# Optimization experiments

Measured on AMD Instinct MI355X. Metric: run time of the kernel, lower is better.

## Reference

```python
import jax, jax.numpy as jnp
import numpy as np

EPS = 1e-6      # delta in ixaxaar/pytorch-dnc util.py and Memory.reset
CLIP = 20.0     # DNC default controller-output clip
M, Wc, R, H, IN, OUT = 10, 20, 1, 256, 27, 128
NN_IN = IN + R * Wc                 # 47 controller input size
IFACE = R * Wc + 3 * Wc + 5 * R + 3  # 88 interface vector size


def _cosine_weights(mem, keys, strengths):
    # mem (B,M,Wc), keys (B,K,Wc), strengths (B,K) -> softmax over cells of scaled cosine sim
    mem_n = mem / (jnp.linalg.norm(mem, axis=2, keepdims=True) + EPS)
    key_n = keys / (jnp.linalg.norm(keys, axis=2, keepdims=True) + EPS)
    d = jnp.einsum('bkw,bmw->bkm', key_n, mem_n)
    return jax.nn.softmax(d * strengths[:, :, None], axis=2)


def _dnc_classifier(x, W_ih, W_hh, b_ih, b_hh, W_xi, b_xi, W_fc, b_fc):
    B, T, _ = x.shape
    # ixaxaar's dnc.py builds inputs[t] = cat(x_t, last_read) ONCE with the initial
    # (zero) last_read, so read vectors never feed the next-step input.
    pad = jnp.zeros((B, R * Wc), x.dtype)
    eye_mask = 1.0 - jnp.eye(M, dtype=x.dtype)

    def step(state, x_t):
        h, c, mem, link, prec, rw, ww, usage = state
        # ---- LSTM controller (1 hidden layer, torch gate order i,f,g,o) ----
        inp = jnp.concatenate([x_t, pad], axis=1)                 # (B,47)
        gates = inp @ W_ih.T + b_ih + h @ W_hh.T + b_hh           # (B,4H)
        i, f, g, o = jnp.split(gates, 4, axis=1)
        c = jax.nn.sigmoid(f) * c + jax.nn.sigmoid(i) * jnp.tanh(g)
        h = jax.nn.sigmoid(o) * jnp.tanh(c)
        out = jnp.clip(h, -CLIP, CLIP)
        # ---- interface vector ----
        xi = out @ W_xi.T + b_xi                                  # (B,88)
        p = R * Wc
        rk = jnp.tanh(xi[:, :p]).reshape(B, R, Wc)                # read keys
        rs = jax.nn.softplus(xi[:, p:p + R]); p += R              # read strengths
        wk = jnp.tanh(xi[:, p:p + Wc]).reshape(B, 1, Wc); p += Wc # write key
        ws = jax.nn.softplus(xi[:, p:p + 1]); p += 1              # write strength
        ev = jax.nn.sigmoid(xi[:, p:p + Wc]); p += Wc             # erase vector
        wv = jnp.tanh(xi[:, p:p + Wc]); p += Wc                   # write vector
        fg = jax.nn.sigmoid(xi[:, p:p + R]); p += R               # free gates
        ag = jax.nn.sigmoid(xi[:, p:p + 1]); p += 1               # allocation gate
        wg = jax.nn.sigmoid(xi[:, p:p + 1]); p += 1               # write gate
        rm = jax.nn.softmax(xi[:, p:p + 3 * R].reshape(B, R, 3), axis=-1)  # read modes (b,f,c)
        # ---- usage (uses PREVIOUS write/read weights) ----
        usage = usage + (1 - usage) * ww
        usage = usage * jnp.prod(1 - fg[:, :, None] * rw, axis=1)
        # ---- write weighting: content + allocation (sort-based free list) ----
        cw = _cosine_weights(mem, wk, ws)[:, 0]                   # (B,M)
        u2 = EPS + (1 - EPS) * usage
        phi = jnp.argsort(u2, axis=1)
        su = jnp.take_along_axis(u2, phi, axis=1)
        prod_excl = jnp.cumprod(jnp.concatenate([jnp.ones((B, 1), u2.dtype), su], axis=1), axis=1)[:, :-1]
        alloc = jnp.take_along_axis((1 - su) * prod_excl, jnp.argsort(phi, axis=1), axis=1)
        ww = wg * (ag * alloc + (1 - ag) * cw)                    # (B,M)
        # ---- erase + write memory ----
        mem = mem * (1 - ww[:, :, None] * ev[:, None, :]) + ww[:, :, None] * wv[:, None, :]
        # ---- temporal link matrix + precedence ----
        link = (1 - ww[:, :, None] - ww[:, None, :]) * link + ww[:, :, None] * prec[:, None, :]
        link = link * eye_mask
        prec = (1 - jnp.sum(ww, axis=1, keepdims=True)) * prec + ww
        # ---- read weighting (content + forward/backward temporal) ----
        cwr = _cosine_weights(mem, rk, rs)                        # (B,R,M)
        fw = jnp.einsum('brm,bnm->brn', rw, link)                 # forward  = L @ w
        bw = jnp.einsum('brm,bmn->brn', rw, link)                 # backward = L^T @ w
        rw = rm[:, :, 0:1] * bw + rm[:, :, 1:2] * fw + rm[:, :, 2:3] * cwr
        return (h, c, mem, link, prec, rw, ww, usage), None

    z = jnp.zeros
    state0 = (z((B, H), x.dtype), z((B, H), x.dtype),
              jnp.full((B, M, Wc), EPS, x.dtype), z((B, M, M), x.dtype),
              z((B, M), x.dtype), jnp.full((B, R, M), EPS, x.dtype),
              jnp.full((B, M), EPS, x.dtype), z((B, M), x.dtype))
    (h, *_), _ = jax.lax.scan(step, state0, jnp.swapaxes(x, 0, 1))
    # classifier head: fc1 on final controller hidden state
    return h @ W_fc.T + b_fc


def setup_inputs() -> dict:
    key = jax.random.key(0)
    ks = jax.random.split(key, 10)
    B, T = 128, 512
    kb = 1.0 / np.sqrt(H)
    u = lambda kk, shape: jax.random.uniform(kk, shape, jnp.float32, -kb, kb)
    return {
        'x': jax.random.normal(ks[0], (B, T, IN), jnp.float32),
        'input_lengths': jax.random.randint(ks[1], (B,), 1, T + 1).astype(jnp.int32),
        'W_ih': u(ks[2], (4 * H, NN_IN)),
        'W_hh': u(ks[3], (4 * H, H)),
        'b_ih': u(ks[4], (4 * H,)),
        'b_hh': u(ks[5], (4 * H,)),
        'W_xi': u(ks[6], (IFACE, H)),
        'b_xi': u(ks[7], (IFACE,)),
        'W_fc': u(ks[8], (OUT, H)),
        'b_fc': u(ks[9], (OUT,)),
    }


def reference(x, input_lengths, W_ih, W_hh, b_ih, b_hh, W_xi, b_xi, W_fc, b_fc):
    # input_lengths is unpacked and discarded by DNCClassifier.forward
    return _dnc_classifier(x, W_ih, W_hh, b_ih, b_hh, W_xi, b_xi, W_fc, b_fc)
```

## Files before the change

kernel.cpp:

```cpp
#include <hip/hip_runtime.h>
#include <hip/hip_fp16.h>


typedef _Float16 h2t __attribute__((ext_vector_type(2)));
typedef unsigned int u32x4 __attribute__((ext_vector_type(4)));

#if defined(__has_builtin)
#  if __has_builtin(__builtin_amdgcn_fdot2)
#    define HAVE_FDOT2 1
#  endif
#endif

__device__ __forceinline__ h2t bc2(unsigned int v) {
  union { unsigned int u; h2t h; } x; x.u = v; return x.h;
}
__device__ __forceinline__ unsigned int pk(float a, float b) {
  union { h2t h; unsigned int u; } x;
  x.h[0] = (_Float16)a; x.h[1] = (_Float16)b;
  return x.u;
}
__device__ __forceinline__ float fdot2f(h2t a, h2t b, float c) {
#ifdef HAVE_FDOT2
  return __builtin_amdgcn_fdot2(a, b, c, false);
#else
  return c + (float)a[0] * (float)b[0] + (float)a[1] * (float)b[1];
#endif
}
__device__ __forceinline__ float dot4(u32x4 w, u32x4 h, float a) {
  a = fdot2f(bc2(w[0]), bc2(h[0]), a);
  a = fdot2f(bc2(w[1]), bc2(h[1]), a);
  a = fdot2f(bc2(w[2]), bc2(h[2]), a);
  a = fdot2f(bc2(w[3]), bc2(h[3]), a);
  return a;
}
__device__ __forceinline__ float sigmf_(float x) {
  return 1.f / (1.f + __expf(-x));
}
__device__ __forceinline__ float tanhf_(float x) {
  float xc = fminf(15.f, fmaxf(-15.f, x));
  float e = __expf(2.f * xc);
  return (e - 1.f) / (e + 1.f);
}

#define WS_P_OFF      0ull
#define WS_WSCAN_OFF  134217728ull
#define WS_WLDS_OFF   134643712ull
#define WS_WSTR_OFF   134725632ull
#define WS_NEED       134742016ull

__global__ void prep_w(const float* __restrict__ W_hh,
                       unsigned char* __restrict__ ws) {
  int idx = blockIdx.x * 256 + threadIdx.x;
  unsigned int* dst; int j, f;
  if (idx < 106496) {
    j = idx; dst = (unsigned int*)(ws + WS_WSCAN_OFF); f = (j >> 2) >> 9;
  } else if (idx < 126976) {
    j = idx - 106496; dst = (unsigned int*)(ws + WS_WLDS_OFF);
    f = 52 + ((j >> 2) >> 9);
  } else {
    j = idx - 126976; dst = (unsigned int*)(ws + WS_WSTR_OFF);
    f = 62 + ((j >> 2) >> 9);
  }
  int e = j & 3, v = (j >> 2) & 511;
  int q = f >> 2, g = f & 3;
  int k2 = ((v >> 8) << 6) + 4 * q + e;
  int r = g * 256 + (v & 255);
  dst[j] = pk(W_hh[r * 256 + 2 * k2], W_hh[r * 256 + 2 * k2 + 1]);
}

__global__ __launch_bounds__(256) void prep_p(const float* __restrict__ x,
                                              const float* __restrict__ W_ih,
                                              const float* __restrict__ b_ih,
                                              const float* __restrict__ b_hh,
                                              unsigned char* __restrict__ ws) {
  __shared__ unsigned int sX[64][14];
  const int u = threadIdx.x;
  const int t = blockIdx.x >> 1;
  const int b0 = (blockIdx.x & 1) << 6;
  unsigned int wih[4][14];
  float bias[4];
#pragma unroll
  for (int g = 0; g < 4; ++g) {
    const float* row = W_ih + (size_t)(g * 256 + u) * 47;
    bias[g] = b_ih[g * 256 + u] + b_hh[g * 256 + u];
#pragma unroll
    for (int j = 0; j < 14; ++j) {
      float a = row[2 * j];
      float b = (2 * j + 1 < 27) ? row[2 * j + 1] : 0.f;
      wih[g][j] = pk(a, b);
    }
  }
#pragma unroll 1
  for (int j = u; j < 896; j += 256) {
    int row = j / 14, c2 = j - 14 * row;
    const float* xr = x + ((size_t)(b0 + row) * 512 + t) * 27;
    float a = xr[2 * c2];
    float bb = (2 * c2 + 1 < 27) ? xr[2 * c2 + 1] : 0.f;
    sX[row][c2] = pk(a, bb);
  }
  __syncthreads();
  uint2* Pout = (uint2*)(ws + WS_P_OFF);
#pragma unroll 2
  for (int p = 0; p < 64; ++p) {
    float a0 = bias[0], a1 = bias[1], a2 = bias[2], a3 = bias[3];
#pragma unroll
    for (int j = 0; j < 14; ++j) {
      h2t xx = bc2(sX[p][j]);
      a0 = fdot2f(bc2(wih[0][j]), xx, a0);
      a1 = fdot2f(bc2(wih[1][j]), xx, a1);
      a2 = fdot2f(bc2(wih[2][j]), xx, a2);
      a3 = fdot2f(bc2(wih[3][j]), xx, a3);
    }
    uint2 o; o.x = pk(a0, a1); o.y = pk(a2, a3);
    Pout[((size_t)t * 128 + (b0 + p)) * 256 + u] = o;
  }
}

__global__ __launch_bounds__(512, 2) void scan_k(
    const unsigned char* __restrict__ ws, const float* __restrict__ W_fc,
    const float* __restrict__ b_fc, float* __restrict__ out) {
  __shared__ u32x4 sWq[10 * 512];
  __shared__ u32x4 sHq[2][32];
  __shared__ float4 sAcc[256];
  __shared__ float sHF[256];
  const int v = threadIdx.x;
  const int b = blockIdx.x;
  const int half = v >> 8;
  const int u = v & 255;

  u32x4 wr[52];
  {
    const u32x4* wsc = (const u32x4*)(ws + WS_WSCAN_OFF);
#pragma unroll
    for (int f = 0; f < 52; ++f) wr[f] = wsc[f * 512 + v];
  }
  {
    const u32x4* wld = (const u32x4*)(ws + WS_WLDS_OFF);
#pragma unroll
    for (int fl = 0; fl < 10; ++fl) sWq[fl * 512 + v] = wld[fl * 512 + v];
  }
  const u32x4* wstr = (const u32x4*)(ws + WS_WSTR_OFF);

  if (v < 64) {
    u32x4 z = {0u, 0u, 0u, 0u};
    ((u32x4*)sHq)[v] = z;
  }
  const uint2* Pbuf = (const uint2*)(ws + WS_P_OFF);
  uint2 pP = make_uint2(0u, 0u);
  if (half == 0) pP = Pbuf[(size_t)b * 256 + u];
  float c = 0.f, hval = 0.f;
  __syncthreads();

#pragma unroll 1
  for (int t = 0; t < 512; ++t) {
    u32x4 tw0 = wstr[0 * 512 + v];
    u32x4 tw1 = wstr[1 * 512 + v];

    const u32x4* rd = &sHq[t & 1][half << 4];
    float acc0 = 0.f, acc1 = 0.f, acc2 = 0.f, acc3 = 0.f;
#pragma unroll
    for (int q = 0; q < 13; ++q) {
      u32x4 hq = rd[q];
      acc0 = dot4(wr[q * 4 + 0], hq, acc0);
      acc1 = dot4(wr[q * 4 + 1], hq, acc1);
      acc2 = dot4(wr[q * 4 + 2], hq, acc2);
      acc3 = dot4(wr[q * 4 + 3], hq, acc3);
    }
    {
      u32x4 hq = rd[13];
      acc0 = dot4(sWq[0 * 512 + v], hq, acc0);
      acc1 = dot4(sWq[1 * 512 + v], hq, acc1);
      acc2 = dot4(sWq[2 * 512 + v], hq, acc2);
      acc3 = dot4(sWq[3 * 512 + v], hq, acc3);
    }
    {
      u32x4 hq = rd[14];
      acc0 = dot4(sWq[4 * 512 + v], hq, acc0);
      acc1 = dot4(sWq[5 * 512 + v], hq, acc1);
      acc2 = dot4(sWq[6 * 512 + v], hq, acc2);
      acc3 = dot4(sWq[7 * 512 + v], hq, acc3);
    }
    {
      u32x4 hq = rd[15];
      acc0 = dot4(sWq[8 * 512 + v], hq, acc0);
      acc1 = dot4(sWq[9 * 512 + v], hq, acc1);
      acc2 = dot4(tw0, hq, acc2);
      acc3 = dot4(tw1, hq, acc3);
    }

    uint2 pPn = pP;
    if (half) {
      sAcc[u] = make_float4(acc0, acc1, acc2, acc3);
    } else {
      int tn = (t < 511) ? (t + 1) : 511;
      pPn = Pbuf[((size_t)tn * 128 + b) * 256 + u];
    }
    __syncthreads();

    if (!half) {
      float4 oth = sAcc[u];
      h2t p01 = bc2(pP.x), p23 = bc2(pP.y);
      float gi = acc0 + oth.x + (float)p01[0];
      float gf = acc1 + oth.y + (float)p01[1];
      float gg = acc2 + oth.z + (float)p23[0];
      float go = acc3 + oth.w + (float)p23[1];
      c = sigmf_(gf) * c + sigmf_(gi) * tanhf_(gg);
      hval = sigmf_(go) * tanhf_(c);
      ((_Float16*)(&sHq[(t + 1) & 1][0]))[u] = (_Float16)hval;
    }
    pP = pPn;
    __syncthreads();
  }

  if (!half) sHF[u] = hval;
  __syncthreads();
  if (v < 128) {
    const float4* wrow = (const float4*)(W_fc + (size_t)v * 256);
    float a = b_fc[v];
#pragma unroll 8
    for (int q = 0; q < 64; ++q) {
      float4 w = wrow[q];
      float4 hh = ((const float4*)sHF)[q];
      a += w.x * hh.x + w.y * hh.y + w.z * hh.z + w.w * hh.w;
    }
    out[(size_t)b * 128 + v] = a;
  }
}

extern "C" void kernel_launch(void* const* d_in, const int* in_sizes, int n_in,
                              void* d_out, int out_size, void* d_ws,
                              size_t ws_size, hipStream_t stream) {
  const float* x    = (const float*)d_in[0];
  const float* W_ih = (const float*)d_in[2];
  const float* W_hh = (const float*)d_in[3];
  const float* b_ih = (const float*)d_in[4];
  const float* b_hh = (const float*)d_in[5];
  const float* W_fc = (const float*)d_in[8];
  const float* b_fc = (const float*)d_in[9];
  unsigned char* ws = (unsigned char*)d_ws;

  if (ws_size < WS_NEED) return;

  prep_w<<<512, 256, 0, stream>>>(W_hh, ws);
  prep_p<<<1024, 256, 0, stream>>>(x, W_ih, b_ih, b_hh, ws);
  scan_k<<<128, 512, 0, stream>>>(ws, W_fc, b_fc, (float*)d_out);
}
```

Before: 876.7 us.

## Split recurrent matvec across 4-lane groups with DPP reduction, one barrier per step

The W_hh weight layout is reorganised so each group of 4 lanes splits the K dimension of the recurrent matvec for two hidden units. Partial sums are then combined with DPP lane shuffles instead of a shared-memory exchange between two half-blocks. This removes one __syncthreads and the sAcc LDS round trip per time step. In exchange, every lane computes the gate nonlinearities redundantly, the P load is no longer prefetched a step ahead, and the h buffer is padded to avoid LDS bank conflicts.

```diff
diff --git a/kernel.cpp b/kernel.cpp
--- a/kernel.cpp
+++ b/kernel.cpp
@@ -40,6 +40,14 @@
   float xc = fminf(15.f, fmaxf(-15.f, x));
   float e = __expf(2.f * xc);
   return (e - 1.f) / (e + 1.f);
+}
+__device__ __forceinline__ float dpp_x1(float x) {
+  return __int_as_float(
+      __builtin_amdgcn_mov_dpp(__float_as_int(x), 0xB1, 0xF, 0xF, true));
+}
+__device__ __forceinline__ float dpp_x2(float x) {
+  return __int_as_float(
+      __builtin_amdgcn_mov_dpp(__float_as_int(x), 0x4E, 0xF, 0xF, true));
 }
 
 #define WS_P_OFF      0ull
@@ -61,11 +69,13 @@
     j = idx - 126976; dst = (unsigned int*)(ws + WS_WSTR_OFF);
     f = 62 + ((j >> 2) >> 9);
   }
-  int e = j & 3, v = (j >> 2) & 511;
-  int q = f >> 2, g = f & 3;
-  int k2 = ((v >> 8) << 6) + 4 * q + e;
-  int r = g * 256 + (v & 255);
-  dst[j] = pk(W_hh[r * 256 + 2 * k2], W_hh[r * 256 + 2 * k2 + 1]);
+  int e = j & 3, vv = (j >> 2) & 511;
+  int w = vv >> 6, l = vv & 63, kq = l & 3, p = l >> 2;
+  int q = f >> 3, uu = (f >> 2) & 1, g = f & 3;
+  int u = w * 32 + 2 * p + uu;
+  int row = g * 256 + u;
+  int k2 = kq * 32 + q * 4 + e;
+  dst[j] = pk(W_hh[row * 256 + 2 * k2], W_hh[row * 256 + 2 * k2 + 1]);
 }
 
 __global__ __launch_bounds__(256) void prep_p(const float* __restrict__ x,
@@ -120,13 +130,15 @@
     const unsigned char* __restrict__ ws, const float* __restrict__ W_fc,
     const float* __restrict__ b_fc, float* __restrict__ out) {
   __shared__ u32x4 sWq[10 * 512];
-  __shared__ u32x4 sHq[2][32];
-  __shared__ float4 sAcc[256];
+  __shared__ __align__(16) unsigned int sH[2][160];
   __shared__ float sHF[256];
   const int v = threadIdx.x;
   const int b = blockIdx.x;
-  const int half = v >> 8;
-  const int u = v & 255;
+  const int l = v & 63;
+  const int w = v >> 6;
+  const int kq = l & 3;
+  const int p = l >> 2;
+  const int u_own = w * 32 + 2 * p + ((l >> 1) & 1);
 
   u32x4 wr[52];
   {
@@ -141,13 +153,11 @@
   }
   const u32x4* wstr = (const u32x4*)(ws + WS_WSTR_OFF);
 
-  if (v < 64) {
-    u32x4 z = {0u, 0u, 0u, 0u};
-    ((u32x4*)sHq)[v] = z;
-  }
+  if (v < 320) ((unsigned int*)sH)[v] = 0u;
   const uint2* Pbuf = (const uint2*)(ws + WS_P_OFF);
-  uint2 pP = make_uint2(0u, 0u);
-  if (half == 0) pP = Pbuf[(size_t)b * 256 + u];
+  const char* hbase = (const char*)sH;
+  char* hwbase = (char*)sH;
+  const int kqoff = kq * 144;
   float c = 0.f, hval = 0.f;
   __syncthreads();
 
@@ -155,73 +165,88 @@
   for (int t = 0; t < 512; ++t) {
     u32x4 tw0 = wstr[0 * 512 + v];
     u32x4 tw1 = wstr[1 * 512 + v];
-
-    const u32x4* rd = &sHq[t & 1][half << 4];
-    float acc0 = 0.f, acc1 = 0.f, acc2 = 0.f, acc3 = 0.f;
-#pragma unroll
-    for (int q = 0; q < 13; ++q) {
-      u32x4 hq = rd[q];
-      acc0 = dot4(wr[q * 4 + 0], hq, acc0);
-      acc1 = dot4(wr[q * 4 + 1], hq, acc1);
-      acc2 = dot4(wr[q * 4 + 2], hq, acc2);
-      acc3 = dot4(wr[q * 4 + 3], hq, acc3);
-    }
-    {
-      u32x4 hq = rd[13];
-      acc0 = dot4(sWq[0 * 512 + v], hq, acc0);
-      acc1 = dot4(sWq[1 * 512 + v], hq, acc1);
-      acc2 = dot4(sWq[2 * 512 + v], hq, acc2);
-      acc3 = dot4(sWq[3 * 512 + v], hq, acc3);
-    }
-    {
-      u32x4 hq = rd[14];
-      acc0 = dot4(sWq[4 * 512 + v], hq, acc0);
-      acc1 = dot4(sWq[5 * 512 + v], hq, acc1);
-      acc2 = dot4(sWq[6 * 512 + v], hq, acc2);
-      acc3 = dot4(sWq[7 * 512 + v], hq, acc3);
-    }
-    {
-      u32x4 hq = rd[15];
-      acc0 = dot4(sWq[8 * 512 + v], hq, acc0);
-      acc1 = dot4(sWq[9 * 512 + v], hq, acc1);
-      acc2 = dot4(tw0, hq, acc2);
-      acc3 = dot4(tw1, hq, acc3);
-    }
-
-    uint2 pPn = pP;
-    if (half) {
-      sAcc[u] = make_float4(acc0, acc1, acc2, acc3);
-    } else {
-      int tn = (t < 511) ? (t + 1) : 511;
-      pPn = Pbuf[((size_t)tn * 128 + b) * 256 + u];
+    uint2 pP = Pbuf[((size_t)t * 128 + b) * 256 + u_own];
+
+    const char* hb = hbase + (t & 1) * 640 + kqoff;
+    float aA0 = 0.f, aA1 = 0.f, aA2 = 0.f, aA3 = 0.f;
+    float aB0 = 0.f, aB1 = 0.f, aB2 = 0.f, aB3 = 0.f;
+    u32x4 hq;
+    hq = *(const u32x4*)(hb + 0);
+    aA0 = dot4(wr[0], hq, aA0);  aA1 = dot4(wr[1], hq, aA1);
+    aA2 = dot4(wr[2], hq, aA2);  aA3 = dot4(wr[3], hq, aA3);
+    aB0 = dot4(wr[4], hq, aB0);  aB1 = dot4(wr[5], hq, aB1);
+    aB2 = dot4(wr[6], hq, aB2);  aB3 = dot4(wr[7], hq, aB3);
+    hq = *(const u32x4*)(hb + 16);
+    aA0 = dot4(wr[8], hq, aA0);  aA1 = dot4(wr[9], hq, aA1);
+    aA2 = dot4(wr[10], hq, aA2); aA3 = dot4(wr[11], hq, aA3);
+    aB0 = dot4(wr[12], hq, aB0); aB1 = dot4(wr[13], hq, aB1);
+    aB2 = dot4(wr[14], hq, aB2); aB3 = dot4(wr[15], hq, aB3);
+    hq = *(const u32x4*)(hb + 32);
+    aA0 = dot4(wr[16], hq, aA0); aA1 = dot4(wr[17], hq, aA1);
+    aA2 = dot4(wr[18], hq, aA2); aA3 = dot4(wr[19], hq, aA3);
+    aB0 = dot4(wr[20], hq, aB0); aB1 = dot4(wr[21], hq, aB1);
+    aB2 = dot4(wr[22], hq, aB2); aB3 = dot4(wr[23], hq, aB3);
+    hq = *(const u32x4*)(hb + 48);
+    aA0 = dot4(wr[24], hq, aA0); aA1 = dot4(wr[25], hq, aA1);
+    aA2 = dot4(wr[26], hq, aA2); aA3 = dot4(wr[27], hq, aA3);
+    aB0 = dot4(wr[28], hq, aB0); aB1 = dot4(wr[29], hq, aB1);
+    aB2 = dot4(wr[30], hq, aB2); aB3 = dot4(wr[31], hq, aB3);
+    hq = *(const u32x4*)(hb + 64);
+    aA0 = dot4(wr[32], hq, aA0); aA1 = dot4(wr[33], hq, aA1);
+    aA2 = dot4(wr[34], hq, aA2); aA3 = dot4(wr[35], hq, aA3);
+    aB0 = dot4(wr[36], hq, aB0); aB1 = dot4(wr[37], hq, aB1);
+    aB2 = dot4(wr[38], hq, aB2); aB3 = dot4(wr[39], hq, aB3);
+    hq = *(const u32x4*)(hb + 80);
+    aA0 = dot4(wr[40], hq, aA0); aA1 = dot4(wr[41], hq, aA1);
+    aA2 = dot4(wr[42], hq, aA2); aA3 = dot4(wr[43], hq, aA3);
+    aB0 = dot4(wr[44], hq, aB0); aB1 = dot4(wr[45], hq, aB1);
+    aB2 = dot4(wr[46], hq, aB2); aB3 = dot4(wr[47], hq, aB3);
+    hq = *(const u32x4*)(hb + 96);
+    aA0 = dot4(wr[48], hq, aA0); aA1 = dot4(wr[49], hq, aA1);
+    aA2 = dot4(wr[50], hq, aA2); aA3 = dot4(wr[51], hq, aA3);
+    aB0 = dot4(sWq[0 * 512 + v], hq, aB0); aB1 = dot4(sWq[1 * 512 + v], hq, aB1);
+    aB2 = dot4(sWq[2 * 512 + v], hq, aB2); aB3 = dot4(sWq[3 * 512 + v], hq, aB3);
+    hq = *(const u32x4*)(hb + 112);
+    aA0 = dot4(sWq[4 * 512 + v], hq, aA0); aA1 = dot4(sWq[5 * 512 + v], hq, aA1);
+    aA2 = dot4(sWq[6 * 512 + v], hq, aA2); aA3 = dot4(sWq[7 * 512 + v], hq, aA3);
+    aB0 = dot4(sWq[8 * 512 + v], hq, aB0); aB1 = dot4(sWq[9 * 512 + v], hq, aB1);
+    aB2 = dot4(tw0, hq, aB2); aB3 = dot4(tw1, hq, aB3);
+
+    aA0 += dpp_x1(aA0); aA0 += dpp_x2(aA0);
+    aA1 += dpp_x1(aA1); aA1 += dpp_x2(aA1);
+    aA2 += dpp_x1(aA2); aA2 += dpp_x2(aA2);
+    aA3 += dpp_x1(aA3); aA3 += dpp_x2(aA3);
+    aB0 += dpp_x1(aB0); aB0 += dpp_x2(aB0);
+    aB1 += dpp_x1(aB1); aB1 += dpp_x2(aB1);
+    aB2 += dpp_x1(aB2); aB2 += dpp_x2(aB2);
+    aB3 += dpp_x1(aB3); aB3 += dpp_x2(aB3);
+
+    float gi = (l & 2) ? aB0 : aA0;
+    float gf = (l & 2) ? aB1 : aA1;
+    float gg = (l & 2) ? aB2 : aA2;
+    float go = (l & 2) ? aB3 : aA3;
+    h2t p01 = bc2(pP.x), p23 = bc2(pP.y);
+    gi += (float)p01[0]; gf += (float)p01[1];
+    gg += (float)p23[0]; go += (float)p23[1];
+    c = sigmf_(gf) * c + sigmf_(gi) * tanhf_(gg);
+    hval = sigmf_(go) * tanhf_(c);
+    if (!(l & 1)) {
+      _Float16* hw = (_Float16*)(hwbase + ((t + 1) & 1) * 640);
+      hw[u_own + (u_own >> 6) * 8] = (_Float16)hval;
     }
     __syncthreads();
-
-    if (!half) {
-      float4 oth = sAcc[u];
-      h2t p01 = bc2(pP.x), p23 = bc2(pP.y);
-      float gi = acc0 + oth.x + (float)p01[0];
-      float gf = acc1 + oth.y + (float)p01[1];
-      float gg = acc2 + oth.z + (float)p23[0];
-      float go = acc3 + oth.w + (float)p23[1];
-      c = sigmf_(gf) * c + sigmf_(gi) * tanhf_(gg);
-      hval = sigmf_(go) * tanhf_(c);
-      ((_Float16*)(&sHq[(t + 1) & 1][0]))[u] = (_Float16)hval;
-    }
-    pP = pPn;
-    __syncthreads();
-  }
-
-  if (!half) sHF[u] = hval;
+  }
+
+  if (!(l & 1)) sHF[u_own] = hval;
   __syncthreads();
   if (v < 128) {
     const float4* wrow = (const float4*)(W_fc + (size_t)v * 256);
     float a = b_fc[v];
 #pragma unroll 8
     for (int q = 0; q < 64; ++q) {
-      float4 w = wrow[q];
+      float4 wq = wrow[q];
       float4 hh = ((const float4*)sHF)[q];
-      a += w.x * hh.x + w.y * hh.y + w.z * hh.z + w.w * hh.w;
+      a += wq.x * hh.x + wq.y * hh.y + wq.z * hh.z + wq.w * hh.w;
     }
     out[(size_t)b * 128 + v] = a;
   }
```

New measurement: 917.9 us. 4.7% more time.
